# Kernel tuning notes

Hardware: AMD Instinct MI355X
Metric: run time of the kernel (lower is better)

The kernel has to match this reference:

```python
import math
import jax, jax.numpy as jnp
import numpy as np

H, W = 512, 512            # volume_shape
N_ANGLES = 360
N_DET = 736                # num_detectors
DET_SPACING = 1.0          # detector_spacing (voxel units)
STEP = 1.0                 # ray-marching step (voxel units)
N_STEPS = int(math.ceil(math.hypot(H, W)))  # 725 samples along each ray


def setup_inputs() -> dict:
    key = jax.random.key(0)
    k1, k2 = jax.random.split(key)
    x = jax.random.normal(k1, (H, W), dtype=jnp.float32)
    # learned reconstruction parameter (zeros in the module; small randn here so the add is non-trivial)
    reco = jax.random.normal(k2, (H, W), dtype=jnp.float32) * 0.1
    angles = jnp.linspace(0.0, np.pi, N_ANGLES, endpoint=False, dtype=jnp.float32)
    return {"x": x, "reco": reco, "angles": angles}


def _bilinear(img, xs, ys):
    """Bilinear interpolation of img[y, x] with zero padding outside."""
    h, w = img.shape
    x0 = jnp.floor(xs)
    y0 = jnp.floor(ys)
    wx = xs - x0
    wy = ys - y0
    x0i = x0.astype(jnp.int32)
    y0i = y0.astype(jnp.int32)

    def fetch(yi, xi):
        inb = (xi >= 0) & (xi < w) & (yi >= 0) & (yi < h)
        v = img[jnp.clip(yi, 0, h - 1), jnp.clip(xi, 0, w - 1)]
        return jnp.where(inb, v, jnp.zeros((), img.dtype))

    return (fetch(y0i, x0i) * (1 - wx) * (1 - wy)
            + fetch(y0i, x0i + 1) * wx * (1 - wy)
            + fetch(y0i + 1, x0i) * (1 - wx) * wy
            + fetch(y0i + 1, x0i + 1) * wx * wy)


def _radon(img, angles):
    """Parallel-beam ray-driven forward projection -> sinogram (n_angles, n_det)."""
    cx = (W - 1) * 0.5
    cy = (H - 1) * 0.5
    u = (jnp.arange(N_DET, dtype=img.dtype) - (N_DET - 1) * 0.5) * DET_SPACING
    t = (jnp.arange(N_STEPS, dtype=img.dtype) - (N_STEPS - 1) * 0.5) * STEP

    def one_angle(theta):
        c = jnp.cos(theta)
        s = jnp.sin(theta)
        # ray: p(t) = u * perp + t * dir, dir = (c, s), perp = (-s, c); centered on volume
        xs = -s * u[:, None] + c * t[None, :] + cx   # (D, T)
        ys = c * u[:, None] + s * t[None, :] + cy    # (D, T)
        return _bilinear(img, xs, ys).sum(axis=1) * STEP  # (D,)

    # lax.map keeps per-angle intermediates small (ray-driven accumulation)
    return jax.lax.map(one_angle, angles)  # (A, D)


def reference(x, reco, angles):
    updated_reco = x + reco
    current_sino = _radon(updated_reco, angles)
    return current_sino, updated_reco
```

## Files before the change

### kernel.cpp

```cpp
#include <hip/hip_runtime.h>
#include <math.h>

constexpr int H = 512, W = 512;
constexpr int N_ANGLES = 360;
constexpr int N_DET = 736;
constexpr int N_STEPS = 725;
constexpr int SINO_SIZE = N_ANGLES * N_DET;

constexpr int DET_TILE = 64;
constexpr int K_TILE   = 64;
constexpr int PITCH    = 100;
constexpr int ROWS     = 93;
constexpr int QCHUNKS  = PITCH / 4;
constexpr int CHUNKS2  = PITCH / 2;
constexpr int MAXJ     = 5;

constexpr int PADX = 96, PADY = 96;
constexpr int PW = 720;
constexpr int PH = 704;
constexpr size_t PAD_BYTES = (size_t)PW * PH * 4;

typedef float v2f __attribute__((ext_vector_type(2)));

__global__ void pad_kernel(const float* __restrict__ x,
                           const float* __restrict__ reco,
                           float* __restrict__ padded,
                           float* __restrict__ updated) {
    int i = blockIdx.x * blockDim.x + threadIdx.x;
    if (i >= PW * PH) return;
    int p = i / PW, q = i - p * PW;
    int gy = p - PADY, gx = q - PADX;
    float v = 0.0f;
    if ((unsigned)gy < (unsigned)H && (unsigned)gx < (unsigned)W) {
        int gi = gy * W + gx;
        v = x[gi] + reco[gi];
        updated[gi] = v;
    }
    padded[i] = v;
}

__global__ void add_kernel(const float4* __restrict__ x,
                           const float4* __restrict__ reco,
                           float4* __restrict__ out) {
    int i = blockIdx.x * blockDim.x + threadIdx.x;
    float4 a = x[i];
    float4 b = reco[i];
    out[i] = make_float4(a.x + b.x, a.y + b.y, a.z + b.z, a.w + b.w);
}

template <bool PADDED>
__global__ __launch_bounds__(512, 8) void radon_kernel(const float* __restrict__ img,
                                                       const float* __restrict__ angles,
                                                       float* __restrict__ sino) {
    __shared__ float tile[ROWS * PITCH];

    const int tid = threadIdx.x;
    const int w   = tid >> 6;
    const int l   = tid & 63;
    const int dt_ = 16 * (w & 3) + (l & 15);
    const int klr = 4 * (w >> 2) + (l >> 4);
    const int a   = blockIdx.y;
    const int d0  = blockIdx.x * DET_TILE;

    const float theta = angles[a];
    const float c = cosf(theta);
    const float s = sinf(theta);
    const float ac = fabsf(c), as = fabsf(s);
    const float cx = (W - 1) * 0.5f;
    const float cy = (H - 1) * 0.5f;
    const float t_off = (N_STEPS - 1) * 0.5f;

    const float u   = (float)(d0 + dt_) - (N_DET - 1) * 0.5f;
    const float bxu = cx - s * u;
    const float byu = cy + c * u;

    const float uLo = (float)d0 - (N_DET - 1) * 0.5f;
    const float uHi = uLo + (DET_TILE - 1);
    float su0 = s * uLo, su1 = s * uHi;
    float smin = fminf(su0, su1), smax = fmaxf(su0, su1);
    float cu0 = c * uLo, cu1 = c * uHi;
    float cmin = fminf(cu0, cu1), cmax = fmaxf(cu0, cu1);

    float tmin = -1e30f, tmax = 1e30f;
    {
        float xlo = -1.0f - cx + smin;
        float xhi = (float)W - cx + smax;
        if (ac > 1e-12f) {
            float t0 = xlo / c, t1 = xhi / c;
            tmin = fmaxf(tmin, fminf(t0, t1));
            tmax = fminf(tmax, fmaxf(t0, t1));
        } else if (xlo > 0.0f || xhi < 0.0f) {
            tmax = -2e30f;
        }
    }
    {
        float ylo = -1.0f - cy - cmax;
        float yhi = (float)H - cy - cmin;
        if (as > 1e-12f) {
            float t0 = ylo / s, t1 = yhi / s;
            tmin = fmaxf(tmin, fminf(t0, t1));
            tmax = fminf(tmax, fmaxf(t0, t1));
        } else if (ylo > 0.0f || yhi < 0.0f) {
            tmax = -2e30f;
        }
    }
    const int kminU = (int)fminf(725.0f, fmaxf(0.0f, ceilf(tmin + t_off) - 1.0f));
    const int kmaxU = (int)fmaxf(-1.0f, fminf((float)(N_STEPS - 1), floorf(tmax + t_off) + 1.0f));

    const float ucf = uLo + 0.5f * (DET_TILE - 1);
    const v2f dinc = {8.0f * c, 8.0f * s};

    float acc = 0.0f;

    for (int k0 = kminU; k0 <= kmaxU; k0 += K_TILE) {
        const int k1 = min(k0 + K_TILE - 1, kmaxU);
        const float t0f = (float)k0 - t_off;
        const float dt  = (float)(k1 - k0);
        const float tc  = t0f + 0.5f * dt;
        const float xc_ = fmaf(c, tc, cx) - s * ucf;
        const float yc_ = fmaf(s, tc, cy) + c * ucf;
        const float hx = fmaf(0.5f * ac, dt, 0.5f * (DET_TILE - 1) * as) + 0.5f;
        const float hy = fmaf(0.5f * as, dt, 0.5f * (DET_TILE - 1) * ac) + 0.5f;
        const int x0 = ((int)floorf(xc_ - hx)) & ~3;
        const int y0 = (int)floorf(yc_ - hy);
        const int bh = min((int)floorf(yc_ + hy) + 1 - y0 + 1, ROWS);

        if constexpr (PADDED) {
            const int total = bh * QCHUNKS;
            const float* srow = img + (size_t)(y0 + PADY) * PW + (x0 + PADX);
            #pragma unroll
            for (int j = 0; j < MAXJ; ++j) {
                const int i = tid + j * 512;
                if (i < total) {
                    const int r  = i / QCHUNKS;
                    const int ch = i - r * QCHUNKS;
                    const float* src = srow + r * PW + ch * 4;
                    float* dst = tile + (size_t)(i & ~63) * 4;
                    __builtin_amdgcn_global_load_lds(
                        (const __attribute__((address_space(1))) unsigned*)src,
                        (__attribute__((address_space(3))) unsigned*)dst,
                        16, 0, 0);
                }
            }
        } else {
            const int total = bh * CHUNKS2;
            for (int i = tid; i < total; i += 512) {
                int r  = i / CHUNKS2;
                int ch = i - r * CHUNKS2;
                int gx = x0 + 2 * ch;
                int gy = y0 + r;
                float2 v = make_float2(0.0f, 0.0f);
                if ((unsigned)gy < (unsigned)H) {
                    const float* rowp = img + gy * W;
                    if (gx >= 0 && gx + 1 < W) {
                        v = *(const float2*)(rowp + gx);
                    } else {
                        if ((unsigned)gx < (unsigned)W)       v.x = rowp[gx];
                        if ((unsigned)(gx + 1) < (unsigned)W) v.y = rowp[gx + 1];
                    }
                }
                *(float2*)(tile + r * PITCH + 2 * ch) = v;
            }
        }
        __syncthreads();

        const int kst = k0 + klr;
        v2f pos = {fmaf(c, (float)kst - t_off, bxu) - (float)x0,
                   fmaf(s, (float)kst - t_off, byu) - (float)y0};
        #pragma unroll 4
        for (int k = kst; k <= k1; k += 8) {
            int xi = (int)pos.x;
            int yi = (int)pos.y;
            float wx = __builtin_amdgcn_fractf(pos.x);
            float wy = __builtin_amdgcn_fractf(pos.y);
            int idx = __mul24(yi, PITCH) + xi;
            v2f c0 = {tile[idx],     tile[idx + PITCH]};
            v2f c1 = {tile[idx + 1], tile[idx + PITCH + 1]};
            v2f diff = c1 - c0;
            v2f wx2 = {wx, wx};
            v2f tb = __builtin_elementwise_fma(wx2, diff, c0);
            acc = fmaf(wy, tb.y - tb.x, acc + tb.x);
            pos += dinc;
        }
        __syncthreads();
    }

    acc += __shfl_xor(acc, 16);
    acc += __shfl_xor(acc, 32);
    float* scratch = tile;
    if (l < 16) scratch[w * 16 + l] = acc;
    __syncthreads();
    if (tid < DET_TILE) {
        int g  = tid >> 4;
        int dd = tid & 15;
        float r = scratch[g * 16 + dd] + scratch[(g + 4) * 16 + dd];
        int dglob = d0 + tid;
        if (dglob < N_DET) sino[a * N_DET + dglob] = r;
    }
}

extern "C" void kernel_launch(void* const* d_in, const int* in_sizes, int n_in,
                              void* d_out, int out_size, void* d_ws, size_t ws_size,
                              hipStream_t stream) {
    const float* x      = (const float*)d_in[0];
    const float* reco   = (const float*)d_in[1];
    const float* angles = (const float*)d_in[2];

    float* sino    = (float*)d_out;
    float* updated = (float*)d_out + SINO_SIZE;

    dim3 grid((N_DET + DET_TILE - 1) / DET_TILE, N_ANGLES);

    if (ws_size >= PAD_BYTES) {
        float* padded = (float*)d_ws;
        pad_kernel<<<(PW * PH + 255) / 256, 256, 0, stream>>>(x, reco, padded, updated);
        radon_kernel<true><<<grid, 512, 0, stream>>>(padded, angles, sino);
    } else {
        int n4 = (H * W) / 4;
        add_kernel<<<n4 / 256, 256, 0, stream>>>(
            (const float4*)x, (const float4*)reco, (float4*)updated);
        radon_kernel<false><<<grid, 512, 0, stream>>>(updated, angles, sino);
    }
}
```

Before: 96.18 us.

## Store image as packed fp16 vertical pairs to halve LDS reads

The padded image now stores, at each pixel, the value and the one below it as a packed pair of fp16 numbers in one 32-bit word. The projection loop can then read a bilinear 2x2 neighbourhood with two LDS loads instead of four. The tile staging is adjusted to match, with one fewer row loaded. The cost is fp16 rounding of the image values, which risks accuracy on the sinogram sums.

```diff
diff --git a/kernel.cpp b/kernel.cpp
--- a/kernel.cpp
+++ b/kernel.cpp
@@ -12,7 +12,6 @@
 constexpr int PITCH    = 100;
 constexpr int ROWS     = 93;
 constexpr int QCHUNKS  = PITCH / 4;
-constexpr int CHUNKS2  = PITCH / 2;
 constexpr int MAXJ     = 5;
 
 constexpr int PADX = 96, PADY = 96;
@@ -21,22 +20,32 @@
 constexpr size_t PAD_BYTES = (size_t)PW * PH * 4;
 
 typedef float v2f __attribute__((ext_vector_type(2)));
+typedef __fp16 h2f __attribute__((ext_vector_type(2)));
+union PackU { unsigned u; h2f h; };
 
 __global__ void pad_kernel(const float* __restrict__ x,
                            const float* __restrict__ reco,
-                           float* __restrict__ padded,
+                           unsigned* __restrict__ padded2,
                            float* __restrict__ updated) {
     int i = blockIdx.x * blockDim.x + threadIdx.x;
     if (i >= PW * PH) return;
     int p = i / PW, q = i - p * PW;
     int gy = p - PADY, gx = q - PADX;
-    float v = 0.0f;
-    if ((unsigned)gy < (unsigned)H && (unsigned)gx < (unsigned)W) {
-        int gi = gy * W + gx;
-        v = x[gi] + reco[gi];
-        updated[gi] = v;
-    }
-    padded[i] = v;
+    float v0 = 0.0f, v1 = 0.0f;
+    if ((unsigned)gx < (unsigned)W) {
+        if ((unsigned)gy < (unsigned)H) {
+            int gi = gy * W + gx;
+            v0 = x[gi] + reco[gi];
+            updated[gi] = v0;
+        }
+        if ((unsigned)(gy + 1) < (unsigned)H) {
+            int gi = (gy + 1) * W + gx;
+            v1 = x[gi] + reco[gi];
+        }
+    }
+    PackU pk;
+    pk.h = __builtin_amdgcn_cvt_pkrtz(v0, v1);
+    padded2[i] = pk.u;
 }
 
 __global__ void add_kernel(const float4* __restrict__ x,
@@ -48,11 +57,11 @@
     out[i] = make_float4(a.x + b.x, a.y + b.y, a.z + b.z, a.w + b.w);
 }
 
-template <bool PADDED>
-__global__ __launch_bounds__(512, 8) void radon_kernel(const float* __restrict__ img,
+template <bool DMA>
+__global__ __launch_bounds__(512, 8) void radon_kernel(const void* __restrict__ imgv,
                                                        const float* __restrict__ angles,
                                                        float* __restrict__ sino) {
-    __shared__ float tile[ROWS * PITCH];
+    __shared__ unsigned tile[ROWS * PITCH];
 
     const int tid = threadIdx.x;
     const int w   = tid >> 6;
@@ -123,19 +132,20 @@
         const float hy = fmaf(0.5f * as, dt, 0.5f * (DET_TILE - 1) * ac) + 0.5f;
         const int x0 = ((int)floorf(xc_ - hx)) & ~3;
         const int y0 = (int)floorf(yc_ - hy);
-        const int bh = min((int)floorf(yc_ + hy) + 1 - y0 + 1, ROWS);
-
-        if constexpr (PADDED) {
+        const int bh = min((int)floorf(yc_ + hy) + 1 - y0, ROWS);
+
+        if constexpr (DMA) {
+            const unsigned* img2 = (const unsigned*)imgv;
             const int total = bh * QCHUNKS;
-            const float* srow = img + (size_t)(y0 + PADY) * PW + (x0 + PADX);
+            const unsigned* srow = img2 + (size_t)(y0 + PADY) * PW + (x0 + PADX);
             #pragma unroll
             for (int j = 0; j < MAXJ; ++j) {
                 const int i = tid + j * 512;
                 if (i < total) {
                     const int r  = i / QCHUNKS;
                     const int ch = i - r * QCHUNKS;
-                    const float* src = srow + r * PW + ch * 4;
-                    float* dst = tile + (size_t)(i & ~63) * 4;
+                    const unsigned* src = srow + r * PW + ch * 4;
+                    unsigned* dst = tile + (size_t)(i & ~63) * 4;
                     __builtin_amdgcn_global_load_lds(
                         (const __attribute__((address_space(1))) unsigned*)src,
                         (__attribute__((address_space(3))) unsigned*)dst,
@@ -143,23 +153,20 @@
                 }
             }
         } else {
-            const int total = bh * CHUNKS2;
+            const float* img = (const float*)imgv;
+            const int total = bh * PITCH;
             for (int i = tid; i < total; i += 512) {
-                int r  = i / CHUNKS2;
-                int ch = i - r * CHUNKS2;
-                int gx = x0 + 2 * ch;
+                int r  = i / PITCH;
+                int gxx = i - r * PITCH + x0;
                 int gy = y0 + r;
-                float2 v = make_float2(0.0f, 0.0f);
-                if ((unsigned)gy < (unsigned)H) {
-                    const float* rowp = img + gy * W;
-                    if (gx >= 0 && gx + 1 < W) {
-                        v = *(const float2*)(rowp + gx);
-                    } else {
-                        if ((unsigned)gx < (unsigned)W)       v.x = rowp[gx];
-                        if ((unsigned)(gx + 1) < (unsigned)W) v.y = rowp[gx + 1];
-                    }
+                float v0 = 0.0f, v1 = 0.0f;
+                if ((unsigned)gxx < (unsigned)W) {
+                    if ((unsigned)gy < (unsigned)H)       v0 = img[gy * W + gxx];
+                    if ((unsigned)(gy + 1) < (unsigned)H) v1 = img[(gy + 1) * W + gxx];
                 }
-                *(float2*)(tile + r * PITCH + 2 * ch) = v;
+                PackU pk;
+                pk.h = __builtin_amdgcn_cvt_pkrtz(v0, v1);
+                tile[i] = pk.u;
             }
         }
         __syncthreads();
@@ -174,8 +181,11 @@
             float wx = __builtin_amdgcn_fractf(pos.x);
             float wy = __builtin_amdgcn_fractf(pos.y);
             int idx = __mul24(yi, PITCH) + xi;
-            v2f c0 = {tile[idx],     tile[idx + PITCH]};
-            v2f c1 = {tile[idx + 1], tile[idx + PITCH + 1]};
+            PackU q0, q1;
+            q0.u = tile[idx];
+            q1.u = tile[idx + 1];
+            v2f c0 = {(float)q0.h.x, (float)q0.h.y};
+            v2f c1 = {(float)q1.h.x, (float)q1.h.y};
             v2f diff = c1 - c0;
             v2f wx2 = {wx, wx};
             v2f tb = __builtin_elementwise_fma(wx2, diff, c0);
@@ -187,7 +197,7 @@
 
     acc += __shfl_xor(acc, 16);
     acc += __shfl_xor(acc, 32);
-    float* scratch = tile;
+    float* scratch = (float*)tile;
     if (l < 16) scratch[w * 16 + l] = acc;
     __syncthreads();
     if (tid < DET_TILE) {
@@ -212,9 +222,9 @@
     dim3 grid((N_DET + DET_TILE - 1) / DET_TILE, N_ANGLES);
 
     if (ws_size >= PAD_BYTES) {
-        float* padded = (float*)d_ws;
-        pad_kernel<<<(PW * PH + 255) / 256, 256, 0, stream>>>(x, reco, padded, updated);
-        radon_kernel<true><<<grid, 512, 0, stream>>>(padded, angles, sino);
+        unsigned* padded2 = (unsigned*)d_ws;
+        pad_kernel<<<(PW * PH + 255) / 256, 256, 0, stream>>>(x, reco, padded2, updated);
+        radon_kernel<true><<<grid, 512, 0, stream>>>(padded2, angles, sino);
     } else {
         int n4 = (H * W) / 4;
         add_kernel<<<n4 / 256, 256, 0, stream>>>(
```

Result: slower. 99.10 us (+3.0%).

## Process two adjacent angles per block sharing one LDS image tile

Applied to the files above, without the earlier changes.

Each block now covers two consecutive projection angles: the k-window and the LDS tile bounding box are taken as the union over both angles, and half the lanes march each angle with step 4 instead of 8. K_TILE shrinks to 56 and ROWS grows to 94 so the union box still fits in the tile, and the tile origin is clamped to the padded image. The goal is to reuse each staged tile for twice the rays and halve the number of tile loads and blocks. The cost is a larger union window, so each tile holds some pixels only one angle needs. The final reduction and sinogram writes change to handle two angles.

```diff
diff --git a/kernel.cpp b/kernel.cpp
--- a/kernel.cpp
+++ b/kernel.cpp
@@ -8,11 +8,11 @@
 constexpr int SINO_SIZE = N_ANGLES * N_DET;
 
 constexpr int DET_TILE = 64;
-constexpr int K_TILE   = 64;
+constexpr int ANG_TILE = 2;
+constexpr int K_TILE   = 56;
 constexpr int PITCH    = 100;
-constexpr int ROWS     = 93;
+constexpr int ROWS     = 94;
 constexpr int QCHUNKS  = PITCH / 4;
-constexpr int CHUNKS2  = PITCH / 2;
 constexpr int MAXJ     = 5;
 
 constexpr int PADX = 96, PADY = 96;
@@ -48,7 +48,7 @@
     out[i] = make_float4(a.x + b.x, a.y + b.y, a.z + b.z, a.w + b.w);
 }
 
-template <bool PADDED>
+template <bool DMA>
 __global__ __launch_bounds__(512, 8) void radon_kernel(const float* __restrict__ img,
                                                        const float* __restrict__ angles,
                                                        float* __restrict__ sino) {
@@ -58,74 +58,104 @@
     const int w   = tid >> 6;
     const int l   = tid & 63;
     const int dt_ = 16 * (w & 3) + (l & 15);
-    const int klr = 4 * (w >> 2) + (l >> 4);
-    const int a   = blockIdx.y;
+    const int al  = (l >> 4) & 1;
+    const int kr  = (l >> 5) + 2 * (w >> 2);
+    const int a0  = blockIdx.y * ANG_TILE;
     const int d0  = blockIdx.x * DET_TILE;
 
-    const float theta = angles[a];
-    const float c = cosf(theta);
-    const float s = sinf(theta);
-    const float ac = fabsf(c), as = fabsf(s);
+    const float th0 = angles[a0];
+    const float th1 = angles[a0 + 1];
+    const float c0a = cosf(th0), s0a = sinf(th0);
+    const float c1a = cosf(th1), s1a = sinf(th1);
     const float cx = (W - 1) * 0.5f;
     const float cy = (H - 1) * 0.5f;
     const float t_off = (N_STEPS - 1) * 0.5f;
 
+    const float c = al ? c1a : c0a;
+    const float s = al ? s1a : s0a;
+
     const float u   = (float)(d0 + dt_) - (N_DET - 1) * 0.5f;
     const float bxu = cx - s * u;
     const float byu = cy + c * u;
 
     const float uLo = (float)d0 - (N_DET - 1) * 0.5f;
     const float uHi = uLo + (DET_TILE - 1);
-    float su0 = s * uLo, su1 = s * uHi;
-    float smin = fminf(su0, su1), smax = fmaxf(su0, su1);
-    float cu0 = c * uLo, cu1 = c * uHi;
-    float cmin = fminf(cu0, cu1), cmax = fmaxf(cu0, cu1);
-
-    float tmin = -1e30f, tmax = 1e30f;
-    {
-        float xlo = -1.0f - cx + smin;
-        float xhi = (float)W - cx + smax;
-        if (ac > 1e-12f) {
-            float t0 = xlo / c, t1 = xhi / c;
-            tmin = fmaxf(tmin, fminf(t0, t1));
-            tmax = fminf(tmax, fmaxf(t0, t1));
-        } else if (xlo > 0.0f || xhi < 0.0f) {
-            tmax = -2e30f;
-        }
-    }
-    {
-        float ylo = -1.0f - cy - cmax;
-        float yhi = (float)H - cy - cmin;
-        if (as > 1e-12f) {
-            float t0 = ylo / s, t1 = yhi / s;
-            tmin = fmaxf(tmin, fminf(t0, t1));
-            tmax = fminf(tmax, fmaxf(t0, t1));
-        } else if (ylo > 0.0f || yhi < 0.0f) {
-            tmax = -2e30f;
-        }
-    }
-    const int kminU = (int)fminf(725.0f, fmaxf(0.0f, ceilf(tmin + t_off) - 1.0f));
-    const int kmaxU = (int)fmaxf(-1.0f, fminf((float)(N_STEPS - 1), floorf(tmax + t_off) + 1.0f));
-
     const float ucf = uLo + 0.5f * (DET_TILE - 1);
-    const v2f dinc = {8.0f * c, 8.0f * s};
+
+    auto windowOf = [&](float ca, float sa, int& kmn, int& kmx) {
+        float aca = fabsf(ca), asa = fabsf(sa);
+        float su0 = sa * uLo, su1 = sa * uHi;
+        float smn = fminf(su0, su1), smx = fmaxf(su0, su1);
+        float cu0 = ca * uLo, cu1 = ca * uHi;
+        float cmn = fminf(cu0, cu1), cmx = fmaxf(cu0, cu1);
+        float tmin = -1e30f, tmax = 1e30f;
+        {
+            float xlo = -1.0f - cx + smn;
+            float xhi = (float)W - cx + smx;
+            if (aca > 1e-12f) {
+                float t0 = xlo / ca, t1 = xhi / ca;
+                tmin = fmaxf(tmin, fminf(t0, t1));
+                tmax = fminf(tmax, fmaxf(t0, t1));
+            } else if (xlo > 0.0f || xhi < 0.0f) {
+                tmax = -2e30f;
+            }
+        }
+        {
+            float ylo = -1.0f - cy - cmx;
+            float yhi = (float)H - cy - cmn;
+            if (asa > 1e-12f) {
+                float t0 = ylo / sa, t1 = yhi / sa;
+                tmin = fmaxf(tmin, fminf(t0, t1));
+                tmax = fminf(tmax, fmaxf(t0, t1));
+            } else if (ylo > 0.0f || yhi < 0.0f) {
+                tmax = -2e30f;
+            }
+        }
+        kmn = (int)fminf(725.0f, fmaxf(0.0f, ceilf(tmin + t_off) - 1.0f));
+        kmx = (int)fmaxf(-1.0f, fminf((float)(N_STEPS - 1), floorf(tmax + t_off) + 1.0f));
+        if (kmn > kmx) { kmn = N_STEPS; kmx = -1; }
+    };
+
+    int kmn0, kmx0, kmn1, kmx1;
+    windowOf(c0a, s0a, kmn0, kmx0);
+    windowOf(c1a, s1a, kmn1, kmx1);
+    const int kminU = min(kmn0, kmn1);
+    const int kmaxU = max(kmx0, kmx1);
+
+    const v2f dinc = {4.0f * c, 4.0f * s};
 
     float acc = 0.0f;
 
     for (int k0 = kminU; k0 <= kmaxU; k0 += K_TILE) {
         const int k1 = min(k0 + K_TILE - 1, kmaxU);
         const float t0f = (float)k0 - t_off;
-        const float dt  = (float)(k1 - k0);
-        const float tc  = t0f + 0.5f * dt;
-        const float xc_ = fmaf(c, tc, cx) - s * ucf;
-        const float yc_ = fmaf(s, tc, cy) + c * ucf;
-        const float hx = fmaf(0.5f * ac, dt, 0.5f * (DET_TILE - 1) * as) + 0.5f;
-        const float hy = fmaf(0.5f * as, dt, 0.5f * (DET_TILE - 1) * ac) + 0.5f;
-        const int x0 = ((int)floorf(xc_ - hx)) & ~3;
-        const int y0 = (int)floorf(yc_ - hy);
-        const int bh = min((int)floorf(yc_ + hy) + 1 - y0 + 1, ROWS);
-
-        if constexpr (PADDED) {
+        const float dtf = (float)(k1 - k0);
+        const float tc  = t0f + 0.5f * dtf;
+
+        float xmn =  1e30f, xmx = -1e30f, ymn = 1e30f, ymx = -1e30f;
+        {
+            float ca = c0a, sa = s0a;
+            #pragma unroll
+            for (int ai = 0; ai < 2; ++ai) {
+                float aca = fabsf(ca), asa = fabsf(sa);
+                float xc_ = fmaf(ca, tc, cx) - sa * ucf;
+                float yc_ = fmaf(sa, tc, cy) + ca * ucf;
+                float hx = fmaf(0.5f * aca, dtf, 0.5f * (DET_TILE - 1) * asa) + 0.5f;
+                float hy = fmaf(0.5f * asa, dtf, 0.5f * (DET_TILE - 1) * aca) + 0.5f;
+                xmn = fminf(xmn, xc_ - hx);
+                xmx = fmaxf(xmx, xc_ + hx);
+                ymn = fminf(ymn, yc_ - hy);
+                ymx = fmaxf(ymx, yc_ + hy);
+                ca = c1a; sa = s1a;
+            }
+        }
+        int x0 = ((int)floorf(xmn)) & ~3;
+        int y0 = (int)floorf(ymn);
+        x0 = min(max(x0, -PADX), PW - PADX - PITCH);
+        y0 = min(max(y0, -PADY), PH - PADY - ROWS);
+        const int bh = min((int)floorf(ymx) + 2 - y0, ROWS);
+
+        if constexpr (DMA) {
             const int total = bh * QCHUNKS;
             const float* srow = img + (size_t)(y0 + PADY) * PW + (x0 + PADX);
             #pragma unroll
@@ -143,59 +173,51 @@
                 }
             }
         } else {
-            const int total = bh * CHUNKS2;
+            const int total = bh * PITCH;
             for (int i = tid; i < total; i += 512) {
-                int r  = i / CHUNKS2;
-                int ch = i - r * CHUNKS2;
-                int gx = x0 + 2 * ch;
+                int r  = i / PITCH;
+                int gxx = i - r * PITCH + x0;
                 int gy = y0 + r;
-                float2 v = make_float2(0.0f, 0.0f);
-                if ((unsigned)gy < (unsigned)H) {
-                    const float* rowp = img + gy * W;
-                    if (gx >= 0 && gx + 1 < W) {
-                        v = *(const float2*)(rowp + gx);
-                    } else {
-                        if ((unsigned)gx < (unsigned)W)       v.x = rowp[gx];
-                        if ((unsigned)(gx + 1) < (unsigned)W) v.y = rowp[gx + 1];
-                    }
-                }
-                *(float2*)(tile + r * PITCH + 2 * ch) = v;
+                float v = 0.0f;
+                if ((unsigned)gxx < (unsigned)W && (unsigned)gy < (unsigned)H)
+                    v = img[gy * W + gxx];
+                tile[i] = v;
             }
         }
         __syncthreads();
 
-        const int kst = k0 + klr;
+        const int kst = k0 + kr;
         v2f pos = {fmaf(c, (float)kst - t_off, bxu) - (float)x0,
                    fmaf(s, (float)kst - t_off, byu) - (float)y0};
         #pragma unroll 4
-        for (int k = kst; k <= k1; k += 8) {
+        for (int k = kst; k <= k1; k += 4) {
             int xi = (int)pos.x;
             int yi = (int)pos.y;
             float wx = __builtin_amdgcn_fractf(pos.x);
             float wy = __builtin_amdgcn_fractf(pos.y);
             int idx = __mul24(yi, PITCH) + xi;
-            v2f c0 = {tile[idx],     tile[idx + PITCH]};
-            v2f c1 = {tile[idx + 1], tile[idx + PITCH + 1]};
-            v2f diff = c1 - c0;
+            v2f cc0 = {tile[idx],     tile[idx + PITCH]};
+            v2f cc1 = {tile[idx + 1], tile[idx + PITCH + 1]};
+            v2f diff = cc1 - cc0;
             v2f wx2 = {wx, wx};
-            v2f tb = __builtin_elementwise_fma(wx2, diff, c0);
+            v2f tb = __builtin_elementwise_fma(wx2, diff, cc0);
             acc = fmaf(wy, tb.y - tb.x, acc + tb.x);
             pos += dinc;
         }
         __syncthreads();
     }
 
-    acc += __shfl_xor(acc, 16);
     acc += __shfl_xor(acc, 32);
     float* scratch = tile;
-    if (l < 16) scratch[w * 16 + l] = acc;
+    if (l < 32) scratch[w * 32 + l] = acc;
     __syncthreads();
-    if (tid < DET_TILE) {
-        int g  = tid >> 4;
-        int dd = tid & 15;
-        float r = scratch[g * 16 + dd] + scratch[(g + 4) * 16 + dd];
-        int dglob = d0 + tid;
-        if (dglob < N_DET) sino[a * N_DET + dglob] = r;
+    if (tid < 128) {
+        int g  = tid >> 5;
+        int ll = tid & 31;
+        float r = scratch[g * 32 + ll] + scratch[(g + 4) * 32 + ll];
+        int d = d0 + 16 * g + (ll & 15);
+        int ang = a0 + ((ll >> 4) & 1);
+        if (d < N_DET) sino[ang * N_DET + d] = r;
     }
 }
 
@@ -209,7 +231,7 @@
     float* sino    = (float*)d_out;
     float* updated = (float*)d_out + SINO_SIZE;
 
-    dim3 grid((N_DET + DET_TILE - 1) / DET_TILE, N_ANGLES);
+    dim3 grid((N_DET + DET_TILE - 1) / DET_TILE, N_ANGLES / ANG_TILE);
 
     if (ws_size >= PAD_BYTES) {
         float* padded = (float*)d_ws;
```

Result: slower. 102.0 us (+6.0%).

## Shrink radon blocks to 256 threads with smaller step tiles

Applied to the files above, without the earlier changes.

Cuts the radon block from 512 to 256 threads and shrinks the ray-step tile from 64 to 32 steps, so the shared-memory tile (rows and pitch) gets smaller and more blocks can be resident. With four waves each covering 16 detectors, the cross-group LDS reduction goes away and results are written straight from the shuffle. It also clamps tile origins to the padded bounds, forces empty ranges when kmin exceeds kmax, and simplifies the non-DMA fallback loader to scalar loads. The trade-off is more tile iterations, each with its own barrier and DMA issue, and more redundant halo loads per step.

```diff
diff --git a/kernel.cpp b/kernel.cpp
--- a/kernel.cpp
+++ b/kernel.cpp
@@ -7,13 +7,13 @@
 constexpr int N_STEPS = 725;
 constexpr int SINO_SIZE = N_ANGLES * N_DET;
 
+constexpr int THREADS  = 256;
 constexpr int DET_TILE = 64;
-constexpr int K_TILE   = 64;
-constexpr int PITCH    = 100;
-constexpr int ROWS     = 93;
+constexpr int K_TILE   = 32;
+constexpr int PITCH    = 84;
+constexpr int ROWS     = 75;
 constexpr int QCHUNKS  = PITCH / 4;
-constexpr int CHUNKS2  = PITCH / 2;
-constexpr int MAXJ     = 5;
+constexpr int MAXJ     = 7;
 
 constexpr int PADX = 96, PADY = 96;
 constexpr int PW = 720;
@@ -48,17 +48,17 @@
     out[i] = make_float4(a.x + b.x, a.y + b.y, a.z + b.z, a.w + b.w);
 }
 
-template <bool PADDED>
-__global__ __launch_bounds__(512, 8) void radon_kernel(const float* __restrict__ img,
-                                                       const float* __restrict__ angles,
-                                                       float* __restrict__ sino) {
+template <bool DMA>
+__global__ __launch_bounds__(THREADS, 6) void radon_kernel(const float* __restrict__ img,
+                                                           const float* __restrict__ angles,
+                                                           float* __restrict__ sino) {
     __shared__ float tile[ROWS * PITCH];
 
     const int tid = threadIdx.x;
     const int w   = tid >> 6;
     const int l   = tid & 63;
-    const int dt_ = 16 * (w & 3) + (l & 15);
-    const int klr = 4 * (w >> 2) + (l >> 4);
+    const int dt_ = 16 * w + (l & 15);
+    const int klr = l >> 4;
     const int a   = blockIdx.y;
     const int d0  = blockIdx.x * DET_TILE;
 
@@ -104,11 +104,12 @@
             tmax = -2e30f;
         }
     }
-    const int kminU = (int)fminf(725.0f, fmaxf(0.0f, ceilf(tmin + t_off) - 1.0f));
-    const int kmaxU = (int)fmaxf(-1.0f, fminf((float)(N_STEPS - 1), floorf(tmax + t_off) + 1.0f));
+    int kminU = (int)fminf(725.0f, fmaxf(0.0f, ceilf(tmin + t_off) - 1.0f));
+    int kmaxU = (int)fmaxf(-1.0f, fminf((float)(N_STEPS - 1), floorf(tmax + t_off) + 1.0f));
+    if (kminU > kmaxU) { kminU = N_STEPS; kmaxU = -1; }
 
     const float ucf = uLo + 0.5f * (DET_TILE - 1);
-    const v2f dinc = {8.0f * c, 8.0f * s};
+    const v2f dinc = {4.0f * c, 4.0f * s};
 
     float acc = 0.0f;
 
@@ -121,16 +122,18 @@
         const float yc_ = fmaf(s, tc, cy) + c * ucf;
         const float hx = fmaf(0.5f * ac, dt, 0.5f * (DET_TILE - 1) * as) + 0.5f;
         const float hy = fmaf(0.5f * as, dt, 0.5f * (DET_TILE - 1) * ac) + 0.5f;
-        const int x0 = ((int)floorf(xc_ - hx)) & ~3;
-        const int y0 = (int)floorf(yc_ - hy);
-        const int bh = min((int)floorf(yc_ + hy) + 1 - y0 + 1, ROWS);
-
-        if constexpr (PADDED) {
+        int x0 = ((int)floorf(xc_ - hx)) & ~3;
+        int y0 = (int)floorf(yc_ - hy);
+        x0 = min(max(x0, -PADX), PW - PADX - PITCH);
+        y0 = min(max(y0, -PADY), PH - PADY - ROWS);
+        const int bh = min((int)floorf(yc_ + hy) + 2 - y0, ROWS);
+
+        if constexpr (DMA) {
             const int total = bh * QCHUNKS;
             const float* srow = img + (size_t)(y0 + PADY) * PW + (x0 + PADX);
             #pragma unroll
             for (int j = 0; j < MAXJ; ++j) {
-                const int i = tid + j * 512;
+                const int i = tid + j * THREADS;
                 if (i < total) {
                     const int r  = i / QCHUNKS;
                     const int ch = i - r * QCHUNKS;
@@ -143,23 +146,15 @@
                 }
             }
         } else {
-            const int total = bh * CHUNKS2;
-            for (int i = tid; i < total; i += 512) {
-                int r  = i / CHUNKS2;
-                int ch = i - r * CHUNKS2;
-                int gx = x0 + 2 * ch;
+            const int total = bh * PITCH;
+            for (int i = tid; i < total; i += THREADS) {
+                int r  = i / PITCH;
+                int gxx = i - r * PITCH + x0;
                 int gy = y0 + r;
-                float2 v = make_float2(0.0f, 0.0f);
-                if ((unsigned)gy < (unsigned)H) {
-                    const float* rowp = img + gy * W;
-                    if (gx >= 0 && gx + 1 < W) {
-                        v = *(const float2*)(rowp + gx);
-                    } else {
-                        if ((unsigned)gx < (unsigned)W)       v.x = rowp[gx];
-                        if ((unsigned)(gx + 1) < (unsigned)W) v.y = rowp[gx + 1];
-                    }
-                }
-                *(float2*)(tile + r * PITCH + 2 * ch) = v;
+                float v = 0.0f;
+                if ((unsigned)gxx < (unsigned)W && (unsigned)gy < (unsigned)H)
+                    v = img[gy * W + gxx];
+                tile[i] = v;
             }
         }
         __syncthreads();
@@ -168,7 +163,7 @@
         v2f pos = {fmaf(c, (float)kst - t_off, bxu) - (float)x0,
                    fmaf(s, (float)kst - t_off, byu) - (float)y0};
         #pragma unroll 4
-        for (int k = kst; k <= k1; k += 8) {
+        for (int k = kst; k <= k1; k += 4) {
             int xi = (int)pos.x;
             int yi = (int)pos.y;
             float wx = __builtin_amdgcn_fractf(pos.x);
@@ -187,15 +182,9 @@
 
     acc += __shfl_xor(acc, 16);
     acc += __shfl_xor(acc, 32);
-    float* scratch = tile;
-    if (l < 16) scratch[w * 16 + l] = acc;
-    __syncthreads();
-    if (tid < DET_TILE) {
-        int g  = tid >> 4;
-        int dd = tid & 15;
-        float r = scratch[g * 16 + dd] + scratch[(g + 4) * 16 + dd];
-        int dglob = d0 + tid;
-        if (dglob < N_DET) sino[a * N_DET + dglob] = r;
+    if (l < 16) {
+        int d = d0 + 16 * w + l;
+        if (d < N_DET) sino[a * N_DET + d] = acc;
     }
 }
 
@@ -214,11 +203,11 @@
     if (ws_size >= PAD_BYTES) {
         float* padded = (float*)d_ws;
         pad_kernel<<<(PW * PH + 255) / 256, 256, 0, stream>>>(x, reco, padded, updated);
-        radon_kernel<true><<<grid, 512, 0, stream>>>(padded, angles, sino);
+        radon_kernel<true><<<grid, THREADS, 0, stream>>>(padded, angles, sino);
     } else {
         int n4 = (H * W) / 4;
         add_kernel<<<n4 / 256, 256, 0, stream>>>(
             (const float4*)x, (const float4*)reco, (float4*)updated);
-        radon_kernel<false><<<grid, 512, 0, stream>>>(updated, angles, sino);
-    }
-}
+        radon_kernel<false><<<grid, THREADS, 0, stream>>>(updated, angles, sino);
+    }
+}
```

After: 101.1 us. 1.05x slower.
